# Kernel tuning notes

Measured on AMD Instinct MI355X. Metric: run time of the kernel, lower is better.

The kernel has to match this reference:

```python
import jax, jax.numpy as jnp
import numpy as np
from jax import lax

HIDDEN = 1024
STATE = 64
BATCH = 16
SEQ = 2048
DT_MIN, DT_MAX = 0.001, 0.1


def setup_inputs() -> dict:
    key = jax.random.key(0)
    k = jax.random.split(key, 6)
    x = jax.random.normal(k[0], (BATCH, SEQ, HIDDEN), dtype=jnp.float32)
    A = jax.random.normal(k[1], (STATE, STATE), dtype=jnp.float32) * 0.01
    B = jax.random.normal(k[2], (STATE, HIDDEN), dtype=jnp.float32) * 0.01
    C = jax.random.normal(k[3], (HIDDEN, STATE), dtype=jnp.float32) * 0.01
    D = jnp.ones((HIDDEN,), dtype=jnp.float32)
    log_dt = jax.random.uniform(k[4], (HIDDEN,), dtype=jnp.float32) * (
        np.log(DT_MAX) - np.log(DT_MIN)
    ) + np.log(DT_MIN)
    return {"x": x, "A": A, "B": B, "C": C, "D": D, "log_dt": log_dt}


def reference(x, A, B, C, D, log_dt):
    # x: (B, T, H)
    dt = jnp.exp(log_dt)                                  # (H,)
    A_bar = jax.scipy.linalg.expm(A * dt.mean())          # (N, N)
    B_bar = B * dt[None, :]                               # (N, H)
    # Precompute input injection for all timesteps: (B, T, N)
    u = jnp.einsum("bth,nh->btn", x, B_bar)

    def step(state, u_t):
        # state: (B, N); u_t: (B, N)
        state = state @ A_bar.T + u_t
        return state, state

    init = jnp.zeros((x.shape[0], A.shape[0]), dtype=x.dtype)
    _, states = lax.scan(step, init, jnp.swapaxes(u, 0, 1))  # (T, B, N)
    states = jnp.swapaxes(states, 0, 1)                      # (B, T, N)
    return jnp.einsum("btn,hn->bth", states, C) + D * x
```

## Files before the change

### kernel.cpp

```cpp
#include <hip/hip_runtime.h>


#define H   1024
#define NS  64
#define NB  16
#define TT  2048
#define LCH 64
#define KCH 32

typedef __attribute__((ext_vector_type(8))) short bf16x8;
typedef __attribute__((ext_vector_type(4))) float f32x4;
typedef __attribute__((ext_vector_type(2))) unsigned int u32x2;

#define WS_ABAR 0
#define WS_AL   4096
#define WS_F    8192
#define WS_P    40960
#define WS_U    73728
#define WS_S    2170880
#define WS_BBF  8192
#define WS_CBF  3219456

__device__ __forceinline__ unsigned short f2bf(float x) {
  union { float f; unsigned u; } v; v.f = x;
  unsigned r = (v.u + 0x7FFFu + ((v.u >> 16) & 1u)) >> 16;
  return (unsigned short)r;
}

__device__ __forceinline__ bf16x8 packbf8(f32x4 a, f32x4 b) {
  bf16x8 r;
  r[0] = (short)f2bf(a[0]); r[1] = (short)f2bf(a[1]);
  r[2] = (short)f2bf(a[2]); r[3] = (short)f2bf(a[3]);
  r[4] = (short)f2bf(b[0]); r[5] = (short)f2bf(b[1]);
  r[6] = (short)f2bf(b[2]); r[7] = (short)f2bf(b[3]);
  return r;
}

__device__ __forceinline__ u32x2 packbf4(f32x4 v) {
  u32x2 r;
  r[0] = (unsigned)f2bf(v[0]) | ((unsigned)f2bf(v[1]) << 16);
  r[1] = (unsigned)f2bf(v[2]) | ((unsigned)f2bf(v[3]) << 16);
  return r;
}

__device__ __forceinline__ f32x4 mfma16(bf16x8 a, bf16x8 b, f32x4 c) {
  return __builtin_amdgcn_mfma_f32_16x16x32_bf16(a, b, c, 0, 0, 0);
}

__global__ __launch_bounds__(256) void k0(const float* Bm, const float* Cm,
                                          const float* ldt, float* ws) {
  short* Bbf = (short*)(ws + WS_BBF);
  short* Cbf = (short*)(ws + WS_CBF);
  const int idx = (blockIdx.x * 256 + threadIdx.x) * 4;
  f32x4 b = *(const f32x4*)(Bm + idx);
  f32x4 l = *(const f32x4*)(ldt + (idx & (H - 1)));
  f32x4 bb;
  for (int j = 0; j < 4; ++j) bb[j] = b[j] * expf(l[j]);
  *(u32x2*)&Bbf[idx] = packbf4(bb);
  f32x4 c = *(const f32x4*)(Cm + idx);
  *(u32x2*)&Cbf[idx] = packbf4(c);
}

__device__ void prep_block(const float* Ain, const float* ldt, float* ws, int which) {
  __shared__ float Mb[64 * 68];
  __shared__ short Tl[64 * 72];
  const int lane = threadIdx.x;
  const int cq = lane >> 4, cl = lane & 15;

  float s = 0.f;
  for (int j = 0; j < 16; ++j) s += expf(ldt[lane + j * 64]);
  for (int off = 32; off; off >>= 1) s += __shfl_down(s, off);
  float dtm = __shfl(s, 0) * (1.0f / 1024.0f);
  float scale = which ? dtm * (float)LCH : dtm;

  for (int idx = lane; idx < 4096; idx += 64) {
    int r = idx >> 6, c = idx & 63;
    float v = Ain[idx] * scale;
    Mb[c * 68 + r] = v;
    Tl[r * 72 + c] = (short)f2bf(v);
  }

  float E[16][4];
  for (int mt = 0; mt < 4; ++mt)
    for (int nt = 0; nt < 4; ++nt)
      for (int r = 0; r < 4; ++r) {
        int row = mt * 16 + cq * 4 + r, col = nt * 16 + cl;
        E[mt * 4 + nt][r] = (row == col ? 1.f : 0.f) + Ain[row * 64 + col] * scale;
      }

  __asm volatile("s_waitcnt lgkmcnt(0)" ::: "memory");

  for (int it = 2; it <= 12; ++it) {
    bf16x8 af[4][2];
    for (int mt = 0; mt < 4; ++mt)
      for (int kh = 0; kh < 2; ++kh)
        af[mt][kh] = *(const bf16x8*)&Tl[(mt * 16 + cl) * 72 + kh * 32 + cq * 8];
    float inv = 1.0f / (float)it;
    bf16x8 bfr[4][2];
    for (int nt = 0; nt < 4; ++nt)
      for (int kh = 0; kh < 2; ++kh) {
        const float* p = &Mb[(nt * 16 + cl) * 68 + kh * 32 + cq * 8];
        f32x4 a = *(const f32x4*)p;
        f32x4 b = *(const f32x4*)(p + 4);
        bfr[nt][kh] = packbf8(a * inv, b * inv);
      }
    f32x4 zero = {0.f, 0.f, 0.f, 0.f};
    f32x4 acc[16];
    for (int i = 0; i < 16; ++i) acc[i] = zero;
    for (int mt = 0; mt < 4; ++mt)
      for (int nt = 0; nt < 4; ++nt) {
        acc[mt * 4 + nt] = mfma16(af[mt][0], bfr[nt][0], acc[mt * 4 + nt]);
        acc[mt * 4 + nt] = mfma16(af[mt][1], bfr[nt][1], acc[mt * 4 + nt]);
      }
    __asm volatile("s_waitcnt lgkmcnt(0)" ::: "memory");
    for (int mt = 0; mt < 4; ++mt)
      for (int nt = 0; nt < 4; ++nt)
        for (int r = 0; r < 4; ++r) {
          float t = acc[mt * 4 + nt][r];
          E[mt * 4 + nt][r] += t;
          Tl[(mt * 16 + cq * 4 + r) * 72 + nt * 16 + cl] = (short)f2bf(t);
        }
    __asm volatile("s_waitcnt lgkmcnt(0)" ::: "memory");
  }

  float* dst = ws + (which ? WS_AL : WS_ABAR);
  for (int mt = 0; mt < 4; ++mt)
    for (int nt = 0; nt < 4; ++nt)
      for (int r = 0; r < 4; ++r)
        dst[(mt * 16 + cq * 4 + r) * 64 + nt * 16 + cl] = E[mt * 4 + nt][r];
}

__device__ void gemm_u(const float* x, const float* ws, float* u2, int bid) {
  const short* Bbf = (const short*)(ws + WS_BBF);
  const int tid = threadIdx.x;
  const int wid = tid >> 6, lane = tid & 63;
  const int cq = lane >> 4, cl = lane & 15;
  const int bt0 = bid * 64 + wid * 16;

  const float* xr = x + (long)(bt0 + cl) * H + cq * 8;
  const short* br = Bbf + cq * 8;

  f32x4 zero = {0.f, 0.f, 0.f, 0.f};
  f32x4 acc[4];
  for (int i = 0; i < 4; ++i) acc[i] = zero;

#pragma unroll 4
  for (int ks = 0; ks < 32; ++ks) {
    const int k0 = ks * 32;
    f32x4 xa = *(const f32x4*)(xr + k0);
    f32x4 xb = *(const f32x4*)(xr + k0 + 4);
    bf16x8 af = packbf8(xa, xb);
    for (int nt = 0; nt < 4; ++nt) {
      bf16x8 bf = *(const bf16x8*)(br + (nt * 16 + cl) * H + k0);
      acc[nt] = mfma16(af, bf, acc[nt]);
    }
  }

  for (int nt = 0; nt < 4; ++nt)
    for (int r = 0; r < 4; ++r) {
      int obt = bt0 + cq * 4 + r;
      int t = obt & (TT - 1), b = obt >> 11;
      u2[(long)(t * 16 + b) * 64 + nt * 16 + cl] = acc[nt][r];
    }
}

__global__ __launch_bounds__(256) void k1(const float* x, const float* Ain,
                                          const float* ldt, float* ws) {
  if (blockIdx.x < 2) {
    if (threadIdx.x < 64) prep_block(Ain, ldt, ws, blockIdx.x);
    return;
  }
  gemm_u(x, ws, ws + WS_U, blockIdx.x - 2);
}

__device__ __forceinline__ void load_RF(const float* Amat, bf16x8 Rf[4][2], int cq, int cl) {
  for (int mt = 0; mt < 4; ++mt)
    for (int kh = 0; kh < 2; ++kh) {
      int m = mt * 16 + cl;
      int kb = kh * 32 + cq * 8;
      f32x4 v0 = *(const f32x4*)&Amat[m * 64 + kb];
      f32x4 v1 = *(const f32x4*)&Amat[m * 64 + kb + 4];
      for (int j = 0; j < 4; ++j) {
        if (m == kb + j) v0[j] -= 1.f;
        if (m == kb + 4 + j) v1[j] -= 1.f;
      }
      Rf[mt][kh] = packbf8(v0, v1);
    }
}

__device__ __forceinline__ void scan_step(f32x4 Z[4], const bf16x8 Rf[4][2], short* Zl,
                                          const f32x4 U[4], int cq, int cl) {
  for (int t = 0; t < 4; ++t)
    *(u32x2*)&Zl[cl * 72 + t * 16 + cq * 4] = packbf4(Z[t]);
  __asm volatile("s_waitcnt lgkmcnt(0)" ::: "memory");
  bf16x8 zf0 = *(const bf16x8*)&Zl[cl * 72 + cq * 8];
  bf16x8 zf1 = *(const bf16x8*)&Zl[cl * 72 + 32 + cq * 8];
  for (int t = 0; t < 4; ++t) Z[t] += U[t];
  for (int mt = 0; mt < 4; ++mt) {
    Z[mt] = mfma16(Rf[mt][0], zf0, Z[mt]);
    Z[mt] = mfma16(Rf[mt][1], zf1, Z[mt]);
  }
}

__global__ __launch_bounds__(64) void scan_local_k(float* ws) {
  const float* Abar = ws + WS_ABAR;
  const float* u2 = ws + WS_U;
  float* F = ws + WS_F;
  __shared__ short Zl[16 * 72];
  const int lane = threadIdx.x, cq = lane >> 4, cl = lane & 15;
  const int c = blockIdx.x;
  bf16x8 Rf[4][2];
  load_RF(Abar, Rf, cq, cl);
  f32x4 zero = {0.f, 0.f, 0.f, 0.f};
  f32x4 Z[4], U[4], Un[4];
  for (int t = 0; t < 4; ++t) Z[t] = zero;
  const float* ub = u2 + (long)c * LCH * 1024 + cl * 64 + cq * 4;
  for (int t = 0; t < 4; ++t) U[t] = *(const f32x4*)(ub + t * 16);
  for (int ti = 0; ti < LCH; ++ti) {
    const float* un = ub + (ti + 1) * 1024;
    for (int t = 0; t < 4; ++t) Un[t] = *(const f32x4*)(un + t * 16);
    scan_step(Z, Rf, Zl, U, cq, cl);
    for (int t = 0; t < 4; ++t) U[t] = Un[t];
  }
  for (int t = 0; t < 4; ++t)
    *(f32x4*)&F[(long)c * 1024 + cl * 64 + t * 16 + cq * 4] = Z[t];
}

__global__ __launch_bounds__(64) void scan_chunks_k(float* ws) {
  const float* AL = ws + WS_AL;
  const float* F = ws + WS_F;
  float* P = ws + WS_P;
  __shared__ short Zl[16 * 72];
  const int lane = threadIdx.x, cq = lane >> 4, cl = lane & 15;
  bf16x8 Rf[4][2];
  load_RF(AL, Rf, cq, cl);
  f32x4 zero = {0.f, 0.f, 0.f, 0.f};
  f32x4 Z[4], U[4];
  for (int t = 0; t < 4; ++t) Z[t] = zero;
  for (int c = 0; c < KCH; ++c) {
    long off = (long)c * 1024 + cl * 64 + cq * 4;
    for (int t = 0; t < 4; ++t) *(f32x4*)&P[off + t * 16] = Z[t];
    for (int t = 0; t < 4; ++t) U[t] = *(const f32x4*)&F[off + t * 16];
    scan_step(Z, Rf, Zl, U, cq, cl);
  }
}

__global__ __launch_bounds__(64) void scan_final_k(float* ws) {
  const float* Abar = ws + WS_ABAR;
  const float* u2 = ws + WS_U;
  const float* P = ws + WS_P;
  short* S2bf = (short*)(ws + WS_S);
  __shared__ short Zl[16 * 72];
  const int lane = threadIdx.x, cq = lane >> 4, cl = lane & 15;
  const int c = blockIdx.x;
  bf16x8 Rf[4][2];
  load_RF(Abar, Rf, cq, cl);
  f32x4 Z[4], U[4], Un[4];
  long poff = (long)c * 1024 + cl * 64 + cq * 4;
  for (int t = 0; t < 4; ++t) Z[t] = *(const f32x4*)&P[poff + t * 16];
  const float* ub = u2 + (long)c * LCH * 1024 + cl * 64 + cq * 4;
  short* sb = S2bf + (long)c * LCH * 1024 + cl * 64 + cq * 4;
  for (int t = 0; t < 4; ++t) U[t] = *(const f32x4*)(ub + t * 16);
  for (int ti = 0; ti < LCH; ++ti) {
    const float* un = ub + (ti + 1) * 1024;
    for (int t = 0; t < 4; ++t) Un[t] = *(const f32x4*)(un + t * 16);
    scan_step(Z, Rf, Zl, U, cq, cl);
    short* so = sb + ti * 1024;
    for (int t = 0; t < 4; ++t) *(u32x2*)(so + t * 16) = packbf4(Z[t]);
    for (int t = 0; t < 4; ++t) U[t] = Un[t];
  }
}

__global__ __launch_bounds__(256) void out_proj_k(const float* ws, const float* Dv,
                                                  const float* x, float* out) {
  const short* Sbf = (const short*)(ws + WS_S);
  const short* Cbf = (const short*)(ws + WS_CBF);
  const int tid = threadIdx.x;
  const int wid = tid >> 6, lane = tid & 63;
  const int cq = lane >> 4, cl = lane & 15;
  const int bid = blockIdx.x;
  const int bt0 = (bid & 511) * 64 + wid * 16;
  const int h0 = (bid >> 9) * 128;

  const int abt = bt0 + cl;
  const int at = abt & (TT - 1), ab = abt >> 11;
  const short* sr = Sbf + (long)(at * 16 + ab) * 64 + cq * 8;
  bf16x8 a0 = *(const bf16x8*)(sr);
  bf16x8 a1 = *(const bf16x8*)(sr + 32);

#pragma unroll
  for (int nt = 0; nt < 8; ++nt) {
    const int h = h0 + nt * 16 + cl;
    const short* cr = Cbf + (long)h * 64 + cq * 8;
    bf16x8 b0 = *(const bf16x8*)(cr);
    bf16x8 b1 = *(const bf16x8*)(cr + 32);
    f32x4 acc = {0.f, 0.f, 0.f, 0.f};
    acc = mfma16(a0, b0, acc);
    acc = mfma16(a1, b1, acc);
    const float d = Dv[h];
    for (int r = 0; r < 4; ++r) {
      long obt = bt0 + cq * 4 + r;
      long idx = obt * H + h;
      out[idx] = acc[r] + d * x[idx];
    }
  }
}

extern "C" void kernel_launch(void* const* d_in, const int* in_sizes, int n_in,
                              void* d_out, int out_size, void* d_ws, size_t ws_size,
                              hipStream_t stream) {
  const float* x = (const float*)d_in[0];
  const float* A = (const float*)d_in[1];
  const float* Bm = (const float*)d_in[2];
  const float* Cm = (const float*)d_in[3];
  const float* Dv = (const float*)d_in[4];
  const float* ldt = (const float*)d_in[5];
  float* out = (float*)d_out;
  float* ws = (float*)d_ws;

  k0<<<dim3(64), dim3(256), 0, stream>>>(Bm, Cm, ldt, ws);
  k1<<<dim3(2 + 512), dim3(256), 0, stream>>>(x, A, ldt, ws);
  scan_local_k<<<dim3(KCH), dim3(64), 0, stream>>>(ws);
  scan_chunks_k<<<dim3(1), dim3(64), 0, stream>>>(ws);
  scan_final_k<<<dim3(KCH), dim3(64), 0, stream>>>(ws);
  out_proj_k<<<dim3(4096), dim3(256), 0, stream>>>(ws, Dv, x, out);
}
```

Before: 507.0 us.

## Fuse all stages into one cooperative kernel with grid-wide syncs

```diff
diff --git a/kernel.cpp b/kernel.cpp
--- a/kernel.cpp
+++ b/kernel.cpp
@@ -1,9 +1,10 @@
 #include <hip/hip_runtime.h>
+#include <hip/hip_cooperative_groups.h>
+
+namespace cg = cooperative_groups;
 
 
 #define H   1024
-#define NS  64
-#define NB  16
 #define TT  2048
 #define LCH 64
 #define KCH 32
@@ -45,20 +46,6 @@
 
 __device__ __forceinline__ f32x4 mfma16(bf16x8 a, bf16x8 b, f32x4 c) {
   return __builtin_amdgcn_mfma_f32_16x16x32_bf16(a, b, c, 0, 0, 0);
-}
-
-__global__ __launch_bounds__(256) void k0(const float* Bm, const float* Cm,
-                                          const float* ldt, float* ws) {
-  short* Bbf = (short*)(ws + WS_BBF);
-  short* Cbf = (short*)(ws + WS_CBF);
-  const int idx = (blockIdx.x * 256 + threadIdx.x) * 4;
-  f32x4 b = *(const f32x4*)(Bm + idx);
-  f32x4 l = *(const f32x4*)(ldt + (idx & (H - 1)));
-  f32x4 bb;
-  for (int j = 0; j < 4; ++j) bb[j] = b[j] * expf(l[j]);
-  *(u32x2*)&Bbf[idx] = packbf4(bb);
-  f32x4 c = *(const f32x4*)(Cm + idx);
-  *(u32x2*)&Cbf[idx] = packbf4(c);
 }
 
 __device__ void prep_block(const float* Ain, const float* ldt, float* ws, int which) {
@@ -130,12 +117,11 @@
         dst[(mt * 16 + cq * 4 + r) * 64 + nt * 16 + cl] = E[mt * 4 + nt][r];
 }
 
-__device__ void gemm_u(const float* x, const float* ws, float* u2, int bid) {
+__device__ void gemm_u_wave(const float* x, const float* ws, float* u2, int w) {
   const short* Bbf = (const short*)(ws + WS_BBF);
-  const int tid = threadIdx.x;
-  const int wid = tid >> 6, lane = tid & 63;
+  const int lane = threadIdx.x & 63;
   const int cq = lane >> 4, cl = lane & 15;
-  const int bt0 = bid * 64 + wid * 16;
+  const int bt0 = w * 16;
 
   const float* xr = x + (long)(bt0 + cl) * H + cq * 8;
   const short* br = Bbf + cq * 8;
@@ -162,15 +148,6 @@
       int t = obt & (TT - 1), b = obt >> 11;
       u2[(long)(t * 16 + b) * 64 + nt * 16 + cl] = acc[nt][r];
     }
-}
-
-__global__ __launch_bounds__(256) void k1(const float* x, const float* Ain,
-                                          const float* ldt, float* ws) {
-  if (blockIdx.x < 2) {
-    if (threadIdx.x < 64) prep_block(Ain, ldt, ws, blockIdx.x);
-    return;
-  }
-  gemm_u(x, ws, ws + WS_U, blockIdx.x - 2);
 }
 
 __device__ __forceinline__ void load_RF(const float* Amat, bf16x8 Rf[4][2], int cq, int cl) {
@@ -202,13 +179,12 @@
   }
 }
 
-__global__ __launch_bounds__(64) void scan_local_k(float* ws) {
+__device__ void scan_local_d(float* ws, int c) {
   const float* Abar = ws + WS_ABAR;
   const float* u2 = ws + WS_U;
   float* F = ws + WS_F;
-  __shared__ short Zl[16 * 72];
-  const int lane = threadIdx.x, cq = lane >> 4, cl = lane & 15;
-  const int c = blockIdx.x;
+  __shared__ short Zl_b[16 * 72];
+  const int lane = threadIdx.x & 63, cq = lane >> 4, cl = lane & 15;
   bf16x8 Rf[4][2];
   load_RF(Abar, Rf, cq, cl);
   f32x4 zero = {0.f, 0.f, 0.f, 0.f};
@@ -219,19 +195,19 @@
   for (int ti = 0; ti < LCH; ++ti) {
     const float* un = ub + (ti + 1) * 1024;
     for (int t = 0; t < 4; ++t) Un[t] = *(const f32x4*)(un + t * 16);
-    scan_step(Z, Rf, Zl, U, cq, cl);
+    scan_step(Z, Rf, Zl_b, U, cq, cl);
     for (int t = 0; t < 4; ++t) U[t] = Un[t];
   }
   for (int t = 0; t < 4; ++t)
     *(f32x4*)&F[(long)c * 1024 + cl * 64 + t * 16 + cq * 4] = Z[t];
 }
 
-__global__ __launch_bounds__(64) void scan_chunks_k(float* ws) {
+__device__ void scan_chunks_d(float* ws) {
   const float* AL = ws + WS_AL;
   const float* F = ws + WS_F;
   float* P = ws + WS_P;
-  __shared__ short Zl[16 * 72];
-  const int lane = threadIdx.x, cq = lane >> 4, cl = lane & 15;
+  __shared__ short Zl_c[16 * 72];
+  const int lane = threadIdx.x & 63, cq = lane >> 4, cl = lane & 15;
   bf16x8 Rf[4][2];
   load_RF(AL, Rf, cq, cl);
   f32x4 zero = {0.f, 0.f, 0.f, 0.f};
@@ -241,18 +217,17 @@
     long off = (long)c * 1024 + cl * 64 + cq * 4;
     for (int t = 0; t < 4; ++t) *(f32x4*)&P[off + t * 16] = Z[t];
     for (int t = 0; t < 4; ++t) U[t] = *(const f32x4*)&F[off + t * 16];
-    scan_step(Z, Rf, Zl, U, cq, cl);
-  }
-}
-
-__global__ __launch_bounds__(64) void scan_final_k(float* ws) {
+    scan_step(Z, Rf, Zl_c, U, cq, cl);
+  }
+}
+
+__device__ void scan_final_d(float* ws, int c) {
   const float* Abar = ws + WS_ABAR;
   const float* u2 = ws + WS_U;
   const float* P = ws + WS_P;
   short* S2bf = (short*)(ws + WS_S);
-  __shared__ short Zl[16 * 72];
-  const int lane = threadIdx.x, cq = lane >> 4, cl = lane & 15;
-  const int c = blockIdx.x;
+  __shared__ short Zl_f[16 * 72];
+  const int lane = threadIdx.x & 63, cq = lane >> 4, cl = lane & 15;
   bf16x8 Rf[4][2];
   load_RF(Abar, Rf, cq, cl);
   f32x4 Z[4], U[4], Un[4];
@@ -264,23 +239,19 @@
   for (int ti = 0; ti < LCH; ++ti) {
     const float* un = ub + (ti + 1) * 1024;
     for (int t = 0; t < 4; ++t) Un[t] = *(const f32x4*)(un + t * 16);
-    scan_step(Z, Rf, Zl, U, cq, cl);
+    scan_step(Z, Rf, Zl_f, U, cq, cl);
     short* so = sb + ti * 1024;
     for (int t = 0; t < 4; ++t) *(u32x2*)(so + t * 16) = packbf4(Z[t]);
     for (int t = 0; t < 4; ++t) U[t] = Un[t];
   }
 }
 
-__global__ __launch_bounds__(256) void out_proj_k(const float* ws, const float* Dv,
-                                                  const float* x, float* out) {
+__device__ void out_wave(const float* ws, const float* Dv, const float* x, float* out, int w) {
   const short* Sbf = (const short*)(ws + WS_S);
   const short* Cbf = (const short*)(ws + WS_CBF);
-  const int tid = threadIdx.x;
-  const int wid = tid >> 6, lane = tid & 63;
+  const int lane = threadIdx.x & 63;
   const int cq = lane >> 4, cl = lane & 15;
-  const int bid = blockIdx.x;
-  const int bt0 = (bid & 511) * 64 + wid * 16;
-  const int h0 = (bid >> 9) * 128;
+  const int bt0 = w * 16;
 
   const int abt = bt0 + cl;
   const int at = abt & (TT - 1), ab = abt >> 11;
@@ -288,22 +259,71 @@
   bf16x8 a0 = *(const bf16x8*)(sr);
   bf16x8 a1 = *(const bf16x8*)(sr + 32);
 
+  for (int hb = 0; hb < 8; ++hb) {
 #pragma unroll
-  for (int nt = 0; nt < 8; ++nt) {
-    const int h = h0 + nt * 16 + cl;
-    const short* cr = Cbf + (long)h * 64 + cq * 8;
-    bf16x8 b0 = *(const bf16x8*)(cr);
-    bf16x8 b1 = *(const bf16x8*)(cr + 32);
-    f32x4 acc = {0.f, 0.f, 0.f, 0.f};
-    acc = mfma16(a0, b0, acc);
-    acc = mfma16(a1, b1, acc);
-    const float d = Dv[h];
-    for (int r = 0; r < 4; ++r) {
-      long obt = bt0 + cq * 4 + r;
-      long idx = obt * H + h;
-      out[idx] = acc[r] + d * x[idx];
-    }
-  }
+    for (int nt = 0; nt < 8; ++nt) {
+      const int h = hb * 128 + nt * 16 + cl;
+      const short* cr = Cbf + (long)h * 64 + cq * 8;
+      bf16x8 b0 = *(const bf16x8*)(cr);
+      bf16x8 b1 = *(const bf16x8*)(cr + 32);
+      f32x4 acc = {0.f, 0.f, 0.f, 0.f};
+      acc = mfma16(a0, b0, acc);
+      acc = mfma16(a1, b1, acc);
+      const float d = Dv[h];
+      for (int r = 0; r < 4; ++r) {
+        long obt = bt0 + cq * 4 + r;
+        long idx = obt * H + h;
+        out[idx] = acc[r] + d * x[idx];
+      }
+    }
+  }
+}
+
+__global__ __launch_bounds__(512, 2) void fused_k(const float* x, const float* Ain,
+                                                  const float* Bm, const float* Cm,
+                                                  const float* Dv, const float* ldt,
+                                                  float* out, float* ws) {
+  cg::grid_group grid = cg::this_grid();
+  const int bid = blockIdx.x, tid = threadIdx.x;
+  const int wid = tid >> 6;
+  const int w = bid * 8 + wid;
+
+  {
+    const int tg = bid * 512 + tid;
+    if (tg < 16384) {
+      short* Bbf = (short*)(ws + WS_BBF);
+      short* Cbf = (short*)(ws + WS_CBF);
+      const int idx = tg * 4;
+      f32x4 b = *(const f32x4*)(Bm + idx);
+      f32x4 l = *(const f32x4*)(ldt + (idx & (H - 1)));
+      f32x4 bb;
+      for (int j = 0; j < 4; ++j) bb[j] = b[j] * expf(l[j]);
+      *(u32x2*)&Bbf[idx] = packbf4(bb);
+      f32x4 c = *(const f32x4*)(Cm + idx);
+      *(u32x2*)&Cbf[idx] = packbf4(c);
+    }
+    if (bid < 2 && wid == 0) prep_block(Ain, ldt, ws, bid);
+  }
+  __threadfence();
+  grid.sync();
+
+  gemm_u_wave(x, ws, ws + WS_U, w);
+  __threadfence();
+  grid.sync();
+
+  if (bid < KCH && wid == 0) scan_local_d(ws, bid);
+  __threadfence();
+  grid.sync();
+
+  if (bid == 0 && wid == 0) scan_chunks_d(ws);
+  __threadfence();
+  grid.sync();
+
+  if (bid < KCH && wid == 0) scan_final_d(ws, bid);
+  __threadfence();
+  grid.sync();
+
+  out_wave(ws, Dv, x, out, w);
 }
 
 extern "C" void kernel_launch(void* const* d_in, const int* in_sizes, int n_in,
@@ -318,10 +338,7 @@
   float* out = (float*)d_out;
   float* ws = (float*)d_ws;
 
-  k0<<<dim3(64), dim3(256), 0, stream>>>(Bm, Cm, ldt, ws);
-  k1<<<dim3(2 + 512), dim3(256), 0, stream>>>(x, A, ldt, ws);
-  scan_local_k<<<dim3(KCH), dim3(64), 0, stream>>>(ws);
-  scan_chunks_k<<<dim3(1), dim3(64), 0, stream>>>(ws);
-  scan_final_k<<<dim3(KCH), dim3(64), 0, stream>>>(ws);
-  out_proj_k<<<dim3(4096), dim3(256), 0, stream>>>(ws, Dv, x, out);
-}
+  void* args[] = {(void*)&x, (void*)&A, (void*)&Bm, (void*)&Cm,
+                  (void*)&Dv, (void*)&ldt, (void*)&out, (void*)&ws};
+  hipLaunchCooperativeKernel((void*)fused_k, dim3(256), dim3(512), args, 0, stream);
+}
```

New measurement: 820.8 us. 1.62x slower.
